# Kernel tuning notes

Hardware: AMD Instinct MI355X
Metric: run time of the kernel (lower is better)

Reference implementation:

```python
import jax, jax.numpy as jnp
import numpy as np

NUM_EMB = 4096
EMB_DIM = 256
COMMIT = 0.25


def setup_inputs() -> dict:
    key = jax.random.key(0)
    k1, k2 = jax.random.split(key)
    z = jax.random.normal(k1, (64, 32, 32, EMB_DIM), dtype=jnp.float32)
    # torch init: uniform(-1/K, 1/K)
    codebook = jax.random.uniform(k2, (NUM_EMB, EMB_DIM), dtype=jnp.float32,
                                  minval=-1.0 / NUM_EMB, maxval=1.0 / NUM_EMB)
    return {"z": z, "codebook": codebook}


def reference(z, codebook):
    zf = z.reshape(-1, EMB_DIM)                       # [N, D]
    # ||z||^2 - 2 z.e + ||e||^2  -> [N, K]
    d = (jnp.sum(zf * zf, axis=1, keepdims=True)
         - 2.0 * (zf @ codebook.T)
         + jnp.sum(codebook * codebook, axis=1))
    idx = jnp.argmin(d, axis=1)                       # [N]
    z_q = codebook[idx].reshape(z.shape)              # gather replaces one-hot matmul
    sg = jax.lax.stop_gradient
    loss = jnp.mean((sg(z_q) - z) ** 2) + COMMIT * jnp.mean((z_q - sg(z)) ** 2)
    z_q_ste = z + sg(z_q - z)                         # straight-through
    return z_q_ste, loss
```

## Files before the change

kernel.cpp:

```cpp
#include <hip/hip_runtime.h>
#include <hip/hip_bf16.h>
#include <stdint.h>

#define NUM_EMB 4096
#define EMB_DIM 256
#define NVEC 65536
#define OUT0_SIZE (NVEC * EMB_DIM)
#define MTILE 128
#define NTILE 64
#define DCONST 0.0625f

typedef __bf16 bf16x8 __attribute__((ext_vector_type(8)));
typedef float floatx16 __attribute__((ext_vector_type(16)));

static __device__ __forceinline__ unsigned int f2bf(float f) {
  unsigned int u = __float_as_uint(f);
  return (u + 0x7fffu + ((u >> 16) & 1u)) >> 16;
}

static __device__ __forceinline__ uint4 pack_bf8(float4 a, float4 b) {
  uint4 r;
  r.x = f2bf(a.x) | (f2bf(a.y) << 16);
  r.y = f2bf(a.z) | (f2bf(a.w) << 16);
  r.z = f2bf(b.x) | (f2bf(b.y) << 16);
  r.w = f2bf(b.z) | (f2bf(b.w) << 16);
  return r;
}

__global__ void __launch_bounds__(256) vq_prep(const float* __restrict__ cbf,
                                               unsigned short* __restrict__ cbb,
                                               float* __restrict__ enorm,
                                               float* __restrict__ out) {
  int w = threadIdx.x >> 6;
  int lane = threadIdx.x & 63;
  int row = blockIdx.x * 4 + w;
  float4 v = ((const float4*)(cbf + (size_t)row * EMB_DIM))[lane];
  float ss = v.x * v.x + v.y * v.y + v.z * v.z + v.w * v.w;
  ushort4 b;
  b.x = (unsigned short)f2bf(v.x);
  b.y = (unsigned short)f2bf(v.y);
  b.z = (unsigned short)f2bf(v.z);
  b.w = (unsigned short)f2bf(v.w);
  ((ushort4*)(cbb + (size_t)row * EMB_DIM))[lane] = b;
#pragma unroll
  for (int m = 1; m < 64; m <<= 1) ss += __shfl_xor(ss, m, 64);
  if (lane == 0) enorm[row] = ss + DCONST;
  if (blockIdx.x == 0 && threadIdx.x == 0) out[OUT0_SIZE] = 0.0f;
}

__global__ void __launch_bounds__(512, 4) vq_main(const float* __restrict__ z,
                                                  const float* __restrict__ cbf,
                                                  const unsigned short* __restrict__ cbb,
                                                  const float* __restrict__ enorm,
                                                  float* __restrict__ out) {
  __shared__ __align__(16) unsigned char sstage[2][NTILE * 512];
  __shared__ unsigned int minlds[2][MTILE];
  __shared__ int idx_lds[MTILE];
  __shared__ float wsum[8];
  __shared__ float zwsum[4];

  const int t = threadIdx.x;
  const int w = t >> 6;
  const int lane = t & 63;
  const int h = lane >> 5;
  const int eL = lane & 31;
  const int rg = w >> 1;
  const int cg = w & 1;
  const int blk = blockIdx.x;
  const int row_base = blk * MTILE + rg * 32;

  auto stage_tile = [&](int buf, int c0) {
#pragma unroll
    for (int j = 0; j < 4; ++j) {
      int e = (w << 3) + (j << 1) + h;
      int s = eL ^ (e & 7);
      const unsigned short* src = cbb + ((size_t)(c0 + e) << 8) + (s << 3);
      __builtin_amdgcn_global_load_lds(
          (const __attribute__((address_space(1))) void*)src,
          (__attribute__((address_space(3))) void*)&sstage[buf][(w << 12) + (j << 10)],
          16, 0, 0);
    }
  };

  stage_tile(0, 0);
  const int laneoff = cg * 32 + eL;

  uint4 afrag[16];
  float zn = 0.f;
  {
    const float* rp = z + (size_t)(row_base + eL) * EMB_DIM + h * 8;
#pragma unroll
    for (int ks = 0; ks < 16; ++ks) {
      float4 a0 = *(const float4*)(rp + ks * 16);
      float4 a1 = *(const float4*)(rp + ks * 16 + 4);
      zn += a0.x * a0.x + a0.y * a0.y + a0.z * a0.z + a0.w * a0.w
          + a1.x * a1.x + a1.y * a1.y + a1.z * a1.z + a1.w * a1.w;
      afrag[ks] = pack_bf8(a0, a1);
    }
    zn += __shfl_xor(zn, 32, 64);
  }
  if (cg == 0) {
    float zs = zn;
#pragma unroll
    for (int m = 1; m <= 16; m <<= 1) zs += __shfl_xor(zs, m, 64);
    if (lane == 0) zwsum[rg] = zs;
  }

  unsigned int pmin[16];
#pragma unroll
  for (int s = 0; s < 16; ++s) pmin[s] = 0xFFFFFFFFu;

  __syncthreads();

  const int sx4 = (eL & 7) << 4;
  int cur = 0;
  float enC = enorm[laneoff];
  for (int c0 = 0; c0 < NUM_EMB; c0 += NTILE) {
    int c1 = c0 + NTILE;
    float enN = enC;
    if (c1 < NUM_EMB) {
      stage_tile(cur ^ 1, c1);
      enN = enorm[c1 + laneoff];
    }

    floatx16 acc;
#pragma unroll
    for (int r = 0; r < 16; ++r) acc[r] = 0.f;
    const unsigned char* bp = &sstage[cur][(size_t)laneoff * 512];
#pragma unroll
    for (int ks = 0; ks < 16; ++ks) {
      uint4 bv = *(const uint4*)(bp + ((ks * 32 + h * 16) ^ sx4));
      bf16x8 b = __builtin_bit_cast(bf16x8, bv);
      acc = __builtin_amdgcn_mfma_f32_32x32x16_bf16(
          __builtin_bit_cast(bf16x8, afrag[ks]), b, acc, 0, 0, 0);
    }

    unsigned int colb = (unsigned int)(c0 + laneoff);
#pragma unroll
    for (int reg = 0; reg < 16; ++reg) {
      float d = fmaf(-2.f, acc[reg], enC);
      unsigned int p = (__float_as_uint(d) & 0xFFFFF000u) | colb;
      pmin[reg] = min(pmin[reg], p);
    }

    __syncthreads();
    cur ^= 1;
    enC = enN;
  }

#pragma unroll
  for (int s = 0; s < 16; ++s) {
    unsigned int v = pmin[s];
#pragma unroll
    for (int m = 1; m <= 16; m <<= 1) {
      unsigned int o = __shfl_xor(v, m, 64);
      if (o < v) v = o;
    }
    pmin[s] = v;
  }
  if (eL == 0) {
#pragma unroll
    for (int s = 0; s < 16; ++s) {
      int rowl = rg * 32 + (s & 3) + 8 * (s >> 2) + 4 * h;
      minlds[cg][rowl] = pmin[s];
    }
  }
  __syncthreads();

  float rl = 0.f;
  if (t < MTILE) {
    unsigned int m0 = minlds[0][t], m1 = minlds[1][t];
    unsigned int m = m1 < m0 ? m1 : m0;
    idx_lds[t] = (int)(m & 0xFFFu);
    rl = __uint_as_float(m & 0xFFFFF000u) - DCONST;
  }
#pragma unroll
  for (int m = 1; m < 64; m <<= 1) rl += __shfl_xor(rl, m, 64);
  if (lane == 0) wsum[w] = rl;
  __syncthreads();
  if (t == 0) {
    float s = ((wsum[0] + wsum[1]) + (wsum[2] + wsum[3]))
            + ((wsum[4] + wsum[5]) + (wsum[6] + wsum[7]))
            + (zwsum[0] + zwsum[1]) + (zwsum[2] + zwsum[3]);
    atomicAdd(out + OUT0_SIZE, s * (1.25f / (float)OUT0_SIZE));
  }

#pragma unroll 4
  for (int j = 0; j < 16; ++j) {
    int id4 = j * 512 + t;
    int r = id4 >> 6, c4 = id4 & 63;
    int k = idx_lds[r];
    float4 ev = ((const float4*)(cbf + (size_t)k * EMB_DIM))[c4];
    ((float4*)(out + (size_t)(blk * MTILE + r) * EMB_DIM))[c4] = ev;
  }
}

extern "C" void kernel_launch(void* const* d_in, const int* in_sizes, int n_in,
                              void* d_out, int out_size, void* d_ws, size_t ws_size,
                              hipStream_t stream) {
  const float* z = (const float*)d_in[0];
  const float* cbf = (const float*)d_in[1];
  unsigned short* cbb = (unsigned short*)d_ws;
  float* enorm = (float*)((char*)d_ws + (size_t)NUM_EMB * EMB_DIM * 2);
  float* out = (float*)d_out;
  vq_prep<<<NUM_EMB / 4, 256, 0, stream>>>(cbf, cbb, enorm, out);
  vq_main<<<NVEC / MTILE, 512, 0, stream>>>(z, cbf, cbb, enorm, out);
}
```

Baseline: 299.4 us.

## Pre-swizzle bf16 codebook into MFMA fragment layout and load directly to registers

The prep kernel now writes the bf16 codebook in a layout that matches the MFMA B-fragment order, so each lane's 16-byte fragment sits contiguously and coalesced. The main loop no longer stages codebook tiles through LDS with global_load_lds and per-tile __syncthreads. Instead it streams fragments straight from global memory (L2-resident) into a 4-deep rotating register buffer, prefetching ahead of each MFMA. This removes LDS traffic and block barriers, but exposes global or L2 latency inside the MFMA loop and adds redundant global reads across waves.

```diff
diff --git a/kernel.cpp b/kernel.cpp
--- a/kernel.cpp
+++ b/kernel.cpp
@@ -18,15 +18,6 @@
   return (u + 0x7fffu + ((u >> 16) & 1u)) >> 16;
 }
 
-static __device__ __forceinline__ uint4 pack_bf8(float4 a, float4 b) {
-  uint4 r;
-  r.x = f2bf(a.x) | (f2bf(a.y) << 16);
-  r.y = f2bf(a.z) | (f2bf(a.w) << 16);
-  r.z = f2bf(b.x) | (f2bf(b.y) << 16);
-  r.w = f2bf(b.z) | (f2bf(b.w) << 16);
-  return r;
-}
-
 __global__ void __launch_bounds__(256) vq_prep(const float* __restrict__ cbf,
                                                unsigned short* __restrict__ cbb,
                                                float* __restrict__ enorm,
@@ -41,7 +32,12 @@
   b.y = (unsigned short)f2bf(v.y);
   b.z = (unsigned short)f2bf(v.z);
   b.w = (unsigned short)f2bf(v.w);
-  ((ushort4*)(cbb + (size_t)row * EMB_DIM))[lane] = b;
+  {
+    int cgrp = row >> 5, eL = row & 31;
+    int ks = lane >> 2, h = (lane >> 1) & 1, q = lane & 1;
+    size_t off16 = (size_t)cgrp * 1024 + ks * 64 + h * 32 + eL;
+    *(ushort4*)((unsigned char*)cbb + off16 * 16 + q * 8) = b;
+  }
 #pragma unroll
   for (int m = 1; m < 64; m <<= 1) ss += __shfl_xor(ss, m, 64);
   if (lane == 0) enorm[row] = ss + DCONST;
@@ -53,7 +49,6 @@
                                                   const unsigned short* __restrict__ cbb,
                                                   const float* __restrict__ enorm,
                                                   float* __restrict__ out) {
-  __shared__ __align__(16) unsigned char sstage[2][NTILE * 512];
   __shared__ unsigned int minlds[2][MTILE];
   __shared__ int idx_lds[MTILE];
   __shared__ float wsum[8];
@@ -69,22 +64,6 @@
   const int blk = blockIdx.x;
   const int row_base = blk * MTILE + rg * 32;
 
-  auto stage_tile = [&](int buf, int c0) {
-#pragma unroll
-    for (int j = 0; j < 4; ++j) {
-      int e = (w << 3) + (j << 1) + h;
-      int s = eL ^ (e & 7);
-      const unsigned short* src = cbb + ((size_t)(c0 + e) << 8) + (s << 3);
-      __builtin_amdgcn_global_load_lds(
-          (const __attribute__((address_space(1))) void*)src,
-          (__attribute__((address_space(3))) void*)&sstage[buf][(w << 12) + (j << 10)],
-          16, 0, 0);
-    }
-  };
-
-  stage_tile(0, 0);
-  const int laneoff = cg * 32 + eL;
-
   uint4 afrag[16];
   float zn = 0.f;
   {
@@ -95,7 +74,12 @@
       float4 a1 = *(const float4*)(rp + ks * 16 + 4);
       zn += a0.x * a0.x + a0.y * a0.y + a0.z * a0.z + a0.w * a0.w
           + a1.x * a1.x + a1.y * a1.y + a1.z * a1.z + a1.w * a1.w;
-      afrag[ks] = pack_bf8(a0, a1);
+      uint4 r;
+      r.x = f2bf(a0.x) | (f2bf(a0.y) << 16);
+      r.y = f2bf(a0.z) | (f2bf(a0.w) << 16);
+      r.z = f2bf(a1.x) | (f2bf(a1.y) << 16);
+      r.w = f2bf(a1.z) | (f2bf(a1.w) << 16);
+      afrag[ks] = r;
     }
     zn += __shfl_xor(zn, 32, 64);
   }
@@ -110,41 +94,43 @@
 #pragma unroll
   for (int s = 0; s < 16; ++s) pmin[s] = 0xFFFFFFFFu;
 
-  __syncthreads();
+  const int lo = h * 32 + eL;
+  const int col = cg * 32 + eL;
+  const uint4* base0 = (const uint4*)cbb + (size_t)cg * 1024 + lo;
+  const uint4* base = base0;
 
-  const int sx4 = (eL & 7) << 4;
-  int cur = 0;
-  float enC = enorm[laneoff];
-  for (int c0 = 0; c0 < NUM_EMB; c0 += NTILE) {
-    int c1 = c0 + NTILE;
-    float enN = enC;
-    if (c1 < NUM_EMB) {
-      stage_tile(cur ^ 1, c1);
-      enN = enorm[c1 + laneoff];
-    }
+  uint4 bw[4];
+#pragma unroll
+  for (int j = 0; j < 4; ++j) bw[j] = base[j * 64];
+
+  float enC = enorm[col];
+  float enN = enC;
+
+  for (int tt = 0; tt < 64; ++tt) {
+    const uint4* nb = (tt < 63) ? (base + 2048) : base0;
+    if (tt < 63) enN = enorm[(tt + 1) * 64 + col];
 
     floatx16 acc;
 #pragma unroll
     for (int r = 0; r < 16; ++r) acc[r] = 0.f;
-    const unsigned char* bp = &sstage[cur][(size_t)laneoff * 512];
+
 #pragma unroll
     for (int ks = 0; ks < 16; ++ks) {
-      uint4 bv = *(const uint4*)(bp + ((ks * 32 + h * 16) ^ sx4));
-      bf16x8 b = __builtin_bit_cast(bf16x8, bv);
+      bf16x8 b = __builtin_bit_cast(bf16x8, bw[ks & 3]);
       acc = __builtin_amdgcn_mfma_f32_32x32x16_bf16(
           __builtin_bit_cast(bf16x8, afrag[ks]), b, acc, 0, 0, 0);
+      bw[ks & 3] = (ks < 12) ? base[(ks + 4) * 64] : nb[(ks - 12) * 64];
     }
 
-    unsigned int colb = (unsigned int)(c0 + laneoff);
+    unsigned int colb = (unsigned int)(tt * 64 + col);
 #pragma unroll
     for (int reg = 0; reg < 16; ++reg) {
       float d = fmaf(-2.f, acc[reg], enC);
-      unsigned int p = (__float_as_uint(d) & 0xFFFFF000u) | colb;
+      unsigned int p = (__float_as_uint(d) & 0xFFFFF000u) | (colb & 0x00000FFFu);
       pmin[reg] = min(pmin[reg], p);
     }
 
-    __syncthreads();
-    cur ^= 1;
+    base = nb;
     enC = enN;
   }
 
```

Result: slower. 404.9 us (+35.2%).
